# Performance work log

Hardware: AMD Instinct MI355X
Metric: run time of the kernel (lower is better)

The kernel has to match this reference:

```python
import jax, jax.numpy as jnp
from jax import lax
import numpy as np

# Keras LSTM cell semantics: gate order [i, f, c(candidate), o];
# recurrent_activation = sigmoid, activation = act (relu for all layers except
# the final decoder LSTM which uses tanh). h = o * act(c).

def lstm_layer(x, W, U, b, act, return_sequences):
    # x: [B, T, I], W: [I, 4H], U: [H, 4H], b: [4H]
    B = x.shape[0]
    H = U.shape[0]
    xW = jnp.einsum('bti,ih->bth', x, W) + b  # precompute input projections
    def step(carry, xw_t):
        h, c = carry
        z = xw_t + h @ U                      # [B, 4H]
        i, f, g, o = jnp.split(z, 4, axis=-1)
        i = jax.nn.sigmoid(i)
        f = jax.nn.sigmoid(f)
        g = act(g)
        o = jax.nn.sigmoid(o)
        c = f * c + i * g
        h = o * act(c)
        return (h, c), h
    h0 = jnp.zeros((B, H), x.dtype)
    (hT, _), hs = lax.scan(step, (h0, h0), jnp.swapaxes(xW, 0, 1))
    if return_sequences:
        return jnp.swapaxes(hs, 0, 1)         # [B, T, H]
    return hT                                  # [B, H]

# layer dims: (in, hidden) for enc0, enc1, enc_latent, dec0, dec1, dec_out
LAYER_DIMS = [(256, 512), (512, 256), (256, 64), (64, 256), (256, 512), (512, 256)]

def setup_inputs() -> dict:
    key = jax.random.key(0)
    keys = jax.random.split(key, 1 + 3 * len(LAYER_DIMS))
    inp = {'x': jax.random.normal(keys[0], (64, 256, 256), dtype=jnp.float32)}
    for li, (din, dh) in enumerate(LAYER_DIMS):
        kw, ku, _ = keys[1 + 3 * li], keys[2 + 3 * li], keys[3 + 3 * li]
        sW = 1.0 / np.sqrt(din)
        sU = 1.0 / np.sqrt(dh)
        inp[f'W{li}'] = jax.random.normal(kw, (din, 4 * dh), dtype=jnp.float32) * sW
        inp[f'U{li}'] = jax.random.normal(ku, (dh, 4 * dh), dtype=jnp.float32) * sU
        inp[f'b{li}'] = jnp.zeros((4 * dh,), dtype=jnp.float32)
    return inp

def reference(x, W0, U0, b0, W1, U1, b1, W2, U2, b2, W3, U3, b3, W4, U4, b4, W5, U5, b5):
    relu = jax.nn.relu
    # encoder: relu LSTMs, all return_sequences=True
    h = lstm_layer(x, W0, U0, b0, relu, True)
    h = lstm_layer(h, W1, U1, b1, relu, True)
    h = lstm_layer(h, W2, U2, b2, relu, True)   # latent_dim=64
    # decoder: relu LSTMs then final tanh LSTM with return_sequences=False
    h = lstm_layer(h, W3, U3, b3, relu, True)
    h = lstm_layer(h, W4, U4, b4, relu, True)
    out = lstm_layer(h, W5, U5, b5, jnp.tanh, False)  # [B, input_size]
    return out
```

## Files before the change

kernel.cpp:

```cpp
#include <hip/hip_runtime.h>
#include <stdint.h>

#define AGENT __HIP_MEMORY_SCOPE_AGENT
typedef unsigned long long u64;

__global__ __launch_bounds__(256) void xpose_in(const float* __restrict__ x,
                                                float* __restrict__ xT) {
  const int t = blockIdx.x;
  const int b = threadIdx.x & 63;
  const int w = threadIdx.x >> 6;
  const float* xr = x + ((size_t)b * 256 + t) * 256;
  float* o = xT + (size_t)t * 256 * 64;
  for (int kq = w * 16; kq < w * 16 + 16; ++kq) {
    float4 v = *(const float4*)(xr + kq * 4);
    o[(size_t)(kq * 4 + 0) * 64 + b] = v.x;
    o[(size_t)(kq * 4 + 1) * 64 + b] = v.y;
    o[(size_t)(kq * 4 + 2) * 64 + b] = v.z;
    o[(size_t)(kq * 4 + 3) * 64 + b] = v.w;
  }
}

__global__ __launch_bounds__(256) void pack_wu(const float* __restrict__ W,
                                               const float* __restrict__ U,
                                               float* __restrict__ out,
                                               int DIN, int H) {
  __shared__ float tile[64][65];
  const int KT = DIN + H;
  const int KTq = KT >> 2;
  const int c0 = blockIdx.x * 64;
  const int k0 = blockIdx.y * 64;
  const int tx = threadIdx.x & 63;
  const int ty = threadIdx.x >> 6;
  for (int r = ty; r < 64; r += 4) {
    const int k = k0 + r;
    tile[r][tx] = (k < DIN) ? W[(size_t)k * (4 * H) + c0 + tx]
                            : U[(size_t)(k - DIN) * (4 * H) + c0 + tx];
  }
  __syncthreads();
  for (int r = ty; r < 64; r += 4) {
    const int cg = c0 + r;
    const int g = cg / H;
    const int col = cg - g * H;
    const int wg = col >> 2;
    const int jl = col & 3;
    const int c = (g << 2) | jl;
    const int k = k0 + tx;
    const int q = k >> 2;
    const int j = k & 3;
    out[(((size_t)wg * KTq + q) * 16 + c) * 4 + j] = tile[tx][r];
  }
}

#define SB __builtin_amdgcn_sched_barrier(0)
#define FMA_K4(A_, W_, M_)                                            \
  A_ = fmaf((W_).x, x0_.M_, A_); A_ = fmaf((W_).y, x1_.M_, A_);       \
  A_ = fmaf((W_).z, x2_.M_, A_); A_ = fmaf((W_).w, x3_.M_, A_);
#define FMA_ROW16(W_, O_)      \
  FMA_K4(acc[(O_) + 0], W_, x) \
  FMA_K4(acc[(O_) + 1], W_, y) \
  FMA_K4(acc[(O_) + 2], W_, z) \
  FMA_K4(acc[(O_) + 3], W_, w)

template <int QW>
__device__ __forceinline__ void accum_cb(const float4* __restrict__ src4,
                                         const float4* __restrict__ wl4,
                                         int bq, int cq4, float acc[16]) {
  static_assert(QW % 4 == 0, "grouping assumes 4|QW");
#pragma unroll 1
  for (int g = 0; g < QW; g += 4) {
#pragma unroll
    for (int ql = g; ql < g + 4; ++ql) {
      const float4 x0_ = src4[(size_t)ql * 64 + 0 * 16 + bq];
      const float4 x1_ = src4[(size_t)ql * 64 + 1 * 16 + bq];
      const float4 x2_ = src4[(size_t)ql * 64 + 2 * 16 + bq];
      const float4 x3_ = src4[(size_t)ql * 64 + 3 * 16 + bq];
      const float4 w0_ = wl4[ql * 16 + cq4 + 0];
      const float4 w1_ = wl4[ql * 16 + cq4 + 1];
      const float4 w2_ = wl4[ql * 16 + cq4 + 2];
      const float4 w3_ = wl4[ql * 16 + cq4 + 3];
      FMA_ROW16(w0_, 0)
      FMA_ROW16(w1_, 4)
      FMA_ROW16(w2_, 8)
      FMA_ROW16(w3_, 12)
    }
    SB;
  }
}

template <int NWG>
__device__ __forceinline__ void agg_body(unsigned* __restrict__ flg,
                                         unsigned* __restrict__ ep) {
  const int tid = threadIdx.x;
  if (tid >= 64) return;
  for (int t = 0; t < 256; ++t) {
    unsigned* base = flg + (size_t)t * NWG;
    if (NWG <= 64) {
      if (tid < NWG) {
        while (__hip_atomic_load(base + tid, __ATOMIC_RELAXED, AGENT) == 0u)
          __builtin_amdgcn_s_sleep(1);
      }
    } else {
      while (__hip_atomic_load(base + tid, __ATOMIC_RELAXED, AGENT) == 0u)
        __builtin_amdgcn_s_sleep(1);
      while (__hip_atomic_load(base + 64 + tid, __ATOMIC_RELAXED, AGENT) == 0u)
        __builtin_amdgcn_s_sleep(1);
    }
    asm volatile("s_waitcnt vmcnt(0)" ::: "memory");
    if (tid == 0)
      __hip_atomic_store(ep, (unsigned)(t + 1), __ATOMIC_RELAXED, AGENT);
  }
}

template <int DIN, int H, int NWG, bool FIN, bool XCOH>
__device__ __forceinline__ void layer_body(
    int wg, int tid, const float* __restrict__ xin, float* __restrict__ hseq,
    const float* __restrict__ wP, const float* __restrict__ bias,
    float* __restrict__ dout, unsigned* __restrict__ selfF,
    unsigned* __restrict__ selfE, unsigned* __restrict__ prevE,
    float* __restrict__ wL, float (*sZ)[16][64], float* sH) {
  constexpr int KT = DIN + H;
  constexpr int KTq = KT / 4;
  constexpr int QX = DIN / 16;
  constexpr int QH = H / 16;
  constexpr int T = 256;
  static_assert(QX % 4 == 0 && QH % 4 == 0, "grouping assumes 4|QW");

  const int lane = tid & 63;
  const int wv = tid >> 6;
  const int bq = lane & 15;
  const int cq4 = (lane >> 4) * 4;

  {
    float4* wl = (float4*)wL;
    const float4* wp = (const float4*)wP + (size_t)wg * KTq * 16;
    for (int i = tid; i < KTq * 16; i += 256) wl[i] = wp[i];
  }
  const float4* wl4x = (const float4*)wL + (size_t)wv * QX * 16;
  const float4* wl4h = (const float4*)wL + ((size_t)(DIN / 4) + wv * QH) * 16;

  float bz[4];
#pragma unroll
  for (int g = 0; g < 4; ++g) bz[g] = bias[g * H + wg * 4 + wv];
  float cst = 0.f;
  __syncthreads();

  for (int t = 0; t < T; ++t) {
    float acc[16];
#pragma unroll
    for (int c = 0; c < 16; ++c) acc[c] = 0.f;

    if (!XCOH) {
      accum_cb<QX>((const float4*)(xin + (size_t)t * DIN * 64) +
                       (size_t)wv * QX * 64,
                   wl4x, bq, cq4, acc);
    }
    if (t > 0 && tid == 0) {
      while (__hip_atomic_load(selfE, __ATOMIC_RELAXED, AGENT) < (unsigned)t)
        __builtin_amdgcn_s_sleep(2);
    }
    if (XCOH && tid == 64) {
      while (__hip_atomic_load(prevE, __ATOMIC_RELAXED, AGENT) <
             (unsigned)(t + 1))
        __builtin_amdgcn_s_sleep(2);
    }
    __syncthreads();
    asm volatile("" ::: "memory");

    if (XCOH) {
      accum_cb<QX>((const float4*)(xin + (size_t)t * DIN * 64) +
                       (size_t)wv * QX * 64,
                   wl4x, bq, cq4, acc);
    }
    if (t > 0) {
      accum_cb<QH>((const float4*)(hseq + (size_t)(t - 1) * H * 64) +
                       (size_t)wv * QH * 64,
                   wl4h, bq, cq4, acc);
    }

#pragma unroll
    for (int i = 0; i < 4; ++i) {
      *(float4*)&sZ[wv][cq4 + i][bq * 4] = make_float4(
          acc[i * 4 + 0], acc[i * 4 + 1], acc[i * 4 + 2], acc[i * 4 + 3]);
    }
    __syncthreads();

    float z[4];
#pragma unroll
    for (int g = 0; g < 4; ++g) {
      z[g] = bz[g];
#pragma unroll
      for (int k = 0; k < 4; ++k) z[g] += sZ[k][g * 4 + wv][lane];
    }
    const float ig = 1.f / (1.f + __expf(-z[0]));
    const float fg = 1.f / (1.f + __expf(-z[1]));
    const float gg = FIN ? tanhf(z[2]) : fmaxf(z[2], 0.f);
    const float og = 1.f / (1.f + __expf(-z[3]));
    cst = fg * cst + ig * gg;
    const float ca = FIN ? tanhf(cst) : fmaxf(cst, 0.f);
    const float h = og * ca;
    sH[lane * 4 + wv] = h;
    if (FIN && t == T - 1) dout[(size_t)lane * H + wg * 4 + wv] = h;
    __syncthreads();

    if (wv == 0) {
      float* hw = hseq + (size_t)t * H * 64 + (size_t)(wg * 4) * 64 + lane;
#pragma unroll
      for (int jl = 0; jl < 4; ++jl) {
        __hip_atomic_store(hw + jl * 64, sH[lane * 4 + jl], __ATOMIC_RELAXED,
                           AGENT);
      }
      asm volatile("s_waitcnt vmcnt(0)" ::: "memory");
      if (tid == 0)
        __hip_atomic_store(&selfF[t * NWG + wg], 1u, __ATOMIC_RELAXED, AGENT);
    }
  }
}

__global__ __launch_bounds__(256, 2) void lstm_fused(
    const float* __restrict__ xT, float* __restrict__ h0,
    float* __restrict__ h1, float* __restrict__ h2, float* __restrict__ h3,
    float* __restrict__ h4, float* __restrict__ h5,
    const float* __restrict__ wuT0, const float* __restrict__ wuT1,
    const float* __restrict__ wuT2, const float* __restrict__ wuT3,
    const float* __restrict__ wuT4, const float* __restrict__ wuT5,
    const float* __restrict__ b0, const float* __restrict__ b1,
    const float* __restrict__ b2, const float* __restrict__ b3,
    const float* __restrict__ b4, const float* __restrict__ b5,
    float* __restrict__ dout, unsigned* __restrict__ f0,
    unsigned* __restrict__ f1, unsigned* __restrict__ f2,
    unsigned* __restrict__ f3, unsigned* __restrict__ f4,
    unsigned* __restrict__ f5, unsigned* __restrict__ eps) {
  __shared__ alignas(16) float wLDS[16 * 768];
  __shared__ alignas(16) float sZ[4][16][64];
  __shared__ alignas(16) float sH[256];
  const int b = blockIdx.x;
  const int tid = threadIdx.x;
  if (b < 128) {
    layer_body<256, 512, 128, false, false>(b, tid, xT, h0, wuT0, b0, nullptr,
                                            f0, eps + 0, nullptr, wLDS, sZ, sH);
  } else if (b < 256) {
    layer_body<256, 512, 128, false, true>(b - 128, tid, h3, h4, wuT4, b4,
                                           nullptr, f4, eps + 4, eps + 3, wLDS,
                                           sZ, sH);
  } else if (b < 320) {
    layer_body<512, 256, 64, false, true>(b - 256, tid, h0, h1, wuT1, b1,
                                          nullptr, f1, eps + 1, eps + 0, wLDS,
                                          sZ, sH);
  } else if (b < 384) {
    layer_body<64, 256, 64, false, true>(b - 320, tid, h2, h3, wuT3, b3,
                                         nullptr, f3, eps + 3, eps + 2, wLDS,
                                         sZ, sH);
  } else if (b < 448) {
    layer_body<512, 256, 64, true, true>(b - 384, tid, h4, h5, wuT5, b5, dout,
                                         f5, eps + 5, eps + 4, wLDS, sZ, sH);
  } else if (b < 464) {
    layer_body<256, 64, 16, false, true>(b - 448, tid, h1, h2, wuT2, b2,
                                         nullptr, f2, eps + 2, eps + 1, wLDS,
                                         sZ, sH);
  } else {
    const int l = b - 464;
    if (l == 0) agg_body<128>(f0, eps + 0);
    else if (l == 1) agg_body<64>(f1, eps + 1);
    else if (l == 2) agg_body<16>(f2, eps + 2);
    else if (l == 3) agg_body<64>(f3, eps + 3);
    else if (l == 4) agg_body<128>(f4, eps + 4);
    else agg_body<64>(f5, eps + 5);
  }
}

extern "C" void kernel_launch(void* const* d_in, const int* in_sizes, int n_in,
                              void* d_out, int out_size, void* d_ws,
                              size_t ws_size, hipStream_t stream) {
  (void)in_sizes; (void)n_in; (void)out_size; (void)ws_size;
  const float* x = (const float*)d_in[0];
  const float* W[6];
  const float* U[6];
  const float* B[6];
  for (int l = 0; l < 6; ++l) {
    W[l] = (const float*)d_in[1 + 3 * l];
    U[l] = (const float*)d_in[2 + 3 * l];
    B[l] = (const float*)d_in[3 + 3 * l];
  }
  char* ws = (char*)d_ws;
  unsigned* f0 = (unsigned*)ws;
  unsigned* f1 = f0 + 128 * 256;
  unsigned* f2 = f1 + 64 * 256;
  unsigned* f3 = f2 + 16 * 256;
  unsigned* f4 = f3 + 64 * 256;
  unsigned* f5 = f4 + 128 * 256;
  unsigned* eps = f0 + 464 * 256;
  float* wuT0 = (float*)(ws + (1u << 20));
  float* wuT1 = wuT0 + (size_t)2048 * 768;
  float* wuT2 = wuT1 + (size_t)1024 * 768;
  float* wuT3 = wuT2 + (size_t)256 * 320;
  float* wuT4 = wuT3 + (size_t)1024 * 320;
  float* wuT5 = wuT4 + (size_t)2048 * 768;
  float* xT = (float*)(ws + (22u << 20));
  float* h0 = (float*)(ws + (38u << 20));
  float* h1 = (float*)(ws + (70u << 20));
  float* h2 = (float*)(ws + (86u << 20));
  float* h3 = (float*)(ws + (90u << 20));
  float* h4 = (float*)(ws + (106u << 20));
  float* h5 = (float*)(ws + (138u << 20));

  hipMemsetAsync(f0, 0, (464 * 256 + 8) * sizeof(unsigned), stream);
  xpose_in<<<256, 256, 0, stream>>>(x, xT);
  pack_wu<<<dim3(32, 12), 256, 0, stream>>>(W[0], U[0], wuT0, 256, 512);
  pack_wu<<<dim3(16, 12), 256, 0, stream>>>(W[1], U[1], wuT1, 512, 256);
  pack_wu<<<dim3(4, 5), 256, 0, stream>>>(W[2], U[2], wuT2, 256, 64);
  pack_wu<<<dim3(16, 5), 256, 0, stream>>>(W[3], U[3], wuT3, 64, 256);
  pack_wu<<<dim3(32, 12), 256, 0, stream>>>(W[4], U[4], wuT4, 256, 512);
  pack_wu<<<dim3(16, 12), 256, 0, stream>>>(W[5], U[5], wuT5, 512, 256);

  lstm_fused<<<470, 256, 0, stream>>>(xT, h0, h1, h2, h3, h4, h5, wuT0, wuT1,
                                      wuT2, wuT3, wuT4, wuT5, B[0], B[1], B[2],
                                      B[3], B[4], B[5], (float*)d_out, f0, f1,
                                      f2, f3, f4, f5, eps);
}
```

Measured before the change: 3.826 ms.

## Double-buffer loads in the accumulation loop and split waits for cross-layer input

```diff
diff --git a/kernel.cpp b/kernel.cpp
--- a/kernel.cpp
+++ b/kernel.cpp
@@ -61,28 +61,46 @@
   FMA_K4(acc[(O_) + 2], W_, z) \
   FMA_K4(acc[(O_) + 3], W_, w)
 
+#define PFX(XB_, S_)                                                      \
+  {                                                                       \
+    _Pragma("unroll") for (int j_ = 0; j_ < 8; ++j_)                      \
+        XB_[j_] =                                                         \
+        src4[(size_t)((S_)*2 + (j_ >> 2)) * 64 + (j_ & 3) * 16 + bq];     \
+  }
+#define PFW(WB_, S_)                                                      \
+  {                                                                       \
+    _Pragma("unroll") for (int j_ = 0; j_ < 8; ++j_)                      \
+        WB_[j_] = wl4[((S_)*2 + (j_ >> 2)) * 16 + cq4 + (j_ & 3)];        \
+  }
+#define FMA2Q(XB_, WB_)                                                   \
+  {                                                                       \
+    {                                                                     \
+      const float4 x0_ = XB_[0], x1_ = XB_[1], x2_ = XB_[2], x3_ = XB_[3];\
+      FMA_ROW16(WB_[0], 0) FMA_ROW16(WB_[1], 4)                           \
+      FMA_ROW16(WB_[2], 8) FMA_ROW16(WB_[3], 12)                          \
+    }                                                                     \
+    {                                                                     \
+      const float4 x0_ = XB_[4], x1_ = XB_[5], x2_ = XB_[6], x3_ = XB_[7];\
+      FMA_ROW16(WB_[4], 0) FMA_ROW16(WB_[5], 4)                           \
+      FMA_ROW16(WB_[6], 8) FMA_ROW16(WB_[7], 12)                          \
+    }                                                                     \
+  }
+
 template <int QW>
 __device__ __forceinline__ void accum_cb(const float4* __restrict__ src4,
                                          const float4* __restrict__ wl4,
                                          int bq, int cq4, float acc[16]) {
-  static_assert(QW % 4 == 0, "grouping assumes 4|QW");
+  static_assert(QW % 4 == 0, "pipeline assumes 4|QW");
+  constexpr int NS = QW / 2;
+  float4 X0[8], X1[8], W0[8], W1[8];
+  PFX(X0, 0) PFW(W0, 0)
 #pragma unroll 1
-  for (int g = 0; g < QW; g += 4) {
-#pragma unroll
-    for (int ql = g; ql < g + 4; ++ql) {
-      const float4 x0_ = src4[(size_t)ql * 64 + 0 * 16 + bq];
-      const float4 x1_ = src4[(size_t)ql * 64 + 1 * 16 + bq];
-      const float4 x2_ = src4[(size_t)ql * 64 + 2 * 16 + bq];
-      const float4 x3_ = src4[(size_t)ql * 64 + 3 * 16 + bq];
-      const float4 w0_ = wl4[ql * 16 + cq4 + 0];
-      const float4 w1_ = wl4[ql * 16 + cq4 + 1];
-      const float4 w2_ = wl4[ql * 16 + cq4 + 2];
-      const float4 w3_ = wl4[ql * 16 + cq4 + 3];
-      FMA_ROW16(w0_, 0)
-      FMA_ROW16(w1_, 4)
-      FMA_ROW16(w2_, 8)
-      FMA_ROW16(w3_, 12)
-    }
+  for (int s = 0; s < NS; s += 2) {
+    PFX(X1, s + 1) PFW(W1, s + 1)
+    FMA2Q(X0, W0)
+    SB;
+    if (s + 2 < NS) { PFX(X0, s + 2) PFW(W0, s + 2) }
+    FMA2Q(X1, W1)
     SB;
   }
 }
@@ -123,7 +141,7 @@
   constexpr int QX = DIN / 16;
   constexpr int QH = H / 16;
   constexpr int T = 256;
-  static_assert(QX % 4 == 0 && QH % 4 == 0, "grouping assumes 4|QW");
+  static_assert(QX % 4 == 0 && QH % 4 == 0, "pipeline assumes 4|QW");
 
   const int lane = tid & 63;
   const int wv = tid >> 6;
@@ -153,24 +171,31 @@
       accum_cb<QX>((const float4*)(xin + (size_t)t * DIN * 64) +
                        (size_t)wv * QX * 64,
                    wl4x, bq, cq4, acc);
-    }
-    if (t > 0 && tid == 0) {
-      while (__hip_atomic_load(selfE, __ATOMIC_RELAXED, AGENT) < (unsigned)t)
-        __builtin_amdgcn_s_sleep(2);
-    }
-    if (XCOH && tid == 64) {
-      while (__hip_atomic_load(prevE, __ATOMIC_RELAXED, AGENT) <
-             (unsigned)(t + 1))
-        __builtin_amdgcn_s_sleep(2);
-    }
-    __syncthreads();
-    asm volatile("" ::: "memory");
-
-    if (XCOH) {
+      if (t > 0 && tid == 0) {
+        while (__hip_atomic_load(selfE, __ATOMIC_RELAXED, AGENT) < (unsigned)t)
+          __builtin_amdgcn_s_sleep(2);
+      }
+      __syncthreads();
+      asm volatile("" ::: "memory");
+    } else {
+      if (tid == 64) {
+        while (__hip_atomic_load(prevE, __ATOMIC_RELAXED, AGENT) <
+               (unsigned)(t + 1))
+          __builtin_amdgcn_s_sleep(2);
+      }
+      __syncthreads();
+      asm volatile("" ::: "memory");
       accum_cb<QX>((const float4*)(xin + (size_t)t * DIN * 64) +
                        (size_t)wv * QX * 64,
                    wl4x, bq, cq4, acc);
-    }
+      if (t > 0 && tid == 0) {
+        while (__hip_atomic_load(selfE, __ATOMIC_RELAXED, AGENT) < (unsigned)t)
+          __builtin_amdgcn_s_sleep(2);
+      }
+      __syncthreads();
+      asm volatile("" ::: "memory");
+    }
+
     if (t > 0) {
       accum_cb<QH>((const float4*)(hseq + (size_t)(t - 1) * H * 64) +
                        (size_t)wv * QH * 64,
```

Measured after the change: 4.079 ms. 6.6% more time.

## Split the per-step K reduction across eight waves with 512-thread blocks

Applied to the files above, without the earlier changes.

```diff
diff --git a/kernel.cpp b/kernel.cpp
--- a/kernel.cpp
+++ b/kernel.cpp
@@ -65,11 +65,12 @@
 __device__ __forceinline__ void accum_cb(const float4* __restrict__ src4,
                                          const float4* __restrict__ wl4,
                                          int bq, int cq4, float acc[16]) {
-  static_assert(QW % 4 == 0, "grouping assumes 4|QW");
+  constexpr int G = (QW % 4 == 0) ? 4 : 2;
+  static_assert(QW % G == 0, "");
 #pragma unroll 1
-  for (int g = 0; g < QW; g += 4) {
-#pragma unroll
-    for (int ql = g; ql < g + 4; ++ql) {
+  for (int g = 0; g < QW; g += G) {
+#pragma unroll
+    for (int ql = g; ql < g + G; ++ql) {
       const float4 x0_ = src4[(size_t)ql * 64 + 0 * 16 + bq];
       const float4 x1_ = src4[(size_t)ql * 64 + 1 * 16 + bq];
       const float4 x2_ = src4[(size_t)ql * 64 + 2 * 16 + bq];
@@ -120,27 +121,29 @@
     float* __restrict__ wL, float (*sZ)[16][64], float* sH) {
   constexpr int KT = DIN + H;
   constexpr int KTq = KT / 4;
-  constexpr int QX = DIN / 16;
-  constexpr int QH = H / 16;
+  constexpr int QX = DIN / 32;
+  constexpr int QH = H / 32;
   constexpr int T = 256;
-  static_assert(QX % 4 == 0 && QH % 4 == 0, "grouping assumes 4|QW");
+  static_assert(QX == 2 || QX % 4 == 0, "");
+  static_assert(QH == 2 || QH % 4 == 0, "");
 
   const int lane = tid & 63;
   const int wv = tid >> 6;
+  const int jw = wv & 3;
   const int bq = lane & 15;
   const int cq4 = (lane >> 4) * 4;
 
   {
     float4* wl = (float4*)wL;
     const float4* wp = (const float4*)wP + (size_t)wg * KTq * 16;
-    for (int i = tid; i < KTq * 16; i += 256) wl[i] = wp[i];
+    for (int i = tid; i < KTq * 16; i += 512) wl[i] = wp[i];
   }
   const float4* wl4x = (const float4*)wL + (size_t)wv * QX * 16;
   const float4* wl4h = (const float4*)wL + ((size_t)(DIN / 4) + wv * QH) * 16;
 
   float bz[4];
 #pragma unroll
-  for (int g = 0; g < 4; ++g) bz[g] = bias[g * H + wg * 4 + wv];
+  for (int g = 0; g < 4; ++g) bz[g] = bias[g * H + wg * 4 + jw];
   float cst = 0.f;
   __syncthreads();
 
@@ -177,29 +180,45 @@
                    wl4h, bq, cq4, acc);
     }
 
-#pragma unroll
-    for (int i = 0; i < 4; ++i) {
-      *(float4*)&sZ[wv][cq4 + i][bq * 4] = make_float4(
-          acc[i * 4 + 0], acc[i * 4 + 1], acc[i * 4 + 2], acc[i * 4 + 3]);
+    if (wv < 4) {
+#pragma unroll
+      for (int i = 0; i < 4; ++i) {
+        *(float4*)&sZ[wv][cq4 + i][bq * 4] = make_float4(
+            acc[i * 4 + 0], acc[i * 4 + 1], acc[i * 4 + 2], acc[i * 4 + 3]);
+      }
     }
     __syncthreads();
-
-    float z[4];
-#pragma unroll
-    for (int g = 0; g < 4; ++g) {
-      z[g] = bz[g];
-#pragma unroll
-      for (int k = 0; k < 4; ++k) z[g] += sZ[k][g * 4 + wv][lane];
-    }
-    const float ig = 1.f / (1.f + __expf(-z[0]));
-    const float fg = 1.f / (1.f + __expf(-z[1]));
-    const float gg = FIN ? tanhf(z[2]) : fmaxf(z[2], 0.f);
-    const float og = 1.f / (1.f + __expf(-z[3]));
-    cst = fg * cst + ig * gg;
-    const float ca = FIN ? tanhf(cst) : fmaxf(cst, 0.f);
-    const float h = og * ca;
-    sH[lane * 4 + wv] = h;
-    if (FIN && t == T - 1) dout[(size_t)lane * H + wg * 4 + wv] = h;
+    if (wv >= 4) {
+#pragma unroll
+      for (int i = 0; i < 4; ++i) {
+        float4 v = *(const float4*)&sZ[wv - 4][cq4 + i][bq * 4];
+        v.x += acc[i * 4 + 0];
+        v.y += acc[i * 4 + 1];
+        v.z += acc[i * 4 + 2];
+        v.w += acc[i * 4 + 3];
+        *(float4*)&sZ[wv - 4][cq4 + i][bq * 4] = v;
+      }
+    }
+    __syncthreads();
+
+    if (wv < 4) {
+      float z[4];
+#pragma unroll
+      for (int g = 0; g < 4; ++g) {
+        z[g] = bz[g];
+#pragma unroll
+        for (int k = 0; k < 4; ++k) z[g] += sZ[k][g * 4 + jw][lane];
+      }
+      const float ig = 1.f / (1.f + __expf(-z[0]));
+      const float fg = 1.f / (1.f + __expf(-z[1]));
+      const float gg = FIN ? tanhf(z[2]) : fmaxf(z[2], 0.f);
+      const float og = 1.f / (1.f + __expf(-z[3]));
+      cst = fg * cst + ig * gg;
+      const float ca = FIN ? tanhf(cst) : fmaxf(cst, 0.f);
+      const float h = og * ca;
+      sH[lane * 4 + jw] = h;
+      if (FIN && t == T - 1) dout[(size_t)lane * H + wg * 4 + jw] = h;
+    }
     __syncthreads();
 
     if (wv == 0) {
@@ -216,7 +235,7 @@
   }
 }
 
-__global__ __launch_bounds__(256, 2) void lstm_fused(
+__global__ __launch_bounds__(512, 4) void lstm_fused(
     const float* __restrict__ xT, float* __restrict__ h0,
     float* __restrict__ h1, float* __restrict__ h2, float* __restrict__ h3,
     float* __restrict__ h4, float* __restrict__ h5,
@@ -312,7 +331,7 @@
   pack_wu<<<dim3(32, 12), 256, 0, stream>>>(W[4], U[4], wuT4, 256, 512);
   pack_wu<<<dim3(16, 12), 256, 0, stream>>>(W[5], U[5], wuT5, 512, 256);
 
-  lstm_fused<<<470, 256, 0, stream>>>(xT, h0, h1, h2, h3, h4, h5, wuT0, wuT1,
+  lstm_fused<<<470, 512, 0, stream>>>(xT, h0, h1, h2, h3, h4, h5, wuT0, wuT1,
                                       wuT2, wuT3, wuT4, wuT5, B[0], B[1], B[2],
                                       B[3], B[4], B[5], (float*)d_out, f0, f1,
                                       f2, f3, f4, f5, eps);
```

Measured after the change: 4.405 ms. 15.1% more time.

## Stage activation chunks into LDS via async global_load_lds triple buffering

Applied to the files above, without the earlier changes.

```diff
diff --git a/kernel.cpp b/kernel.cpp
--- a/kernel.cpp
+++ b/kernel.cpp
@@ -61,29 +61,60 @@
   FMA_K4(acc[(O_) + 2], W_, z) \
   FMA_K4(acc[(O_) + 3], W_, w)
 
+typedef const __attribute__((address_space(1))) void* gas_t;
+typedef __attribute__((address_space(3))) void* las_t;
+#define GLDS(G_, L_) \
+  __builtin_amdgcn_global_load_lds((gas_t)(const void*)(G_), \
+                                   (las_t)(void*)(L_), 16, 0, 0)
+#define STAGE2(C_, P_)                                            \
+  {                                                               \
+    const float4* g_ = src4 + (size_t)(C_)*128 + lane;            \
+    float* l_ = xb + (P_)*512;                                    \
+    GLDS(g_, l_);                                                 \
+    GLDS(g_ + 64, l_ + 256);                                      \
+  }
+
 template <int QW>
-__device__ __forceinline__ void accum_cb(const float4* __restrict__ src4,
-                                         const float4* __restrict__ wl4,
-                                         int bq, int cq4, float acc[16]) {
-  static_assert(QW % 4 == 0, "grouping assumes 4|QW");
+__device__ __forceinline__ void accum_lds(const float4* __restrict__ src4,
+                                          float* __restrict__ xb,
+                                          const float4* __restrict__ wl4,
+                                          int lane, int bq, int cq4,
+                                          float acc[16]) {
+  static_assert(QW % 2 == 0 && QW >= 4, "");
+  constexpr int NC = QW / 2;
+  STAGE2(0, 0)
+  STAGE2(1, 1)
+  int pc = 0, pn = 2;
 #pragma unroll 1
-  for (int g = 0; g < QW; g += 4) {
-#pragma unroll
-    for (int ql = g; ql < g + 4; ++ql) {
-      const float4 x0_ = src4[(size_t)ql * 64 + 0 * 16 + bq];
-      const float4 x1_ = src4[(size_t)ql * 64 + 1 * 16 + bq];
-      const float4 x2_ = src4[(size_t)ql * 64 + 2 * 16 + bq];
-      const float4 x3_ = src4[(size_t)ql * 64 + 3 * 16 + bq];
-      const float4 w0_ = wl4[ql * 16 + cq4 + 0];
-      const float4 w1_ = wl4[ql * 16 + cq4 + 1];
-      const float4 w2_ = wl4[ql * 16 + cq4 + 2];
-      const float4 w3_ = wl4[ql * 16 + cq4 + 3];
+  for (int c = 0; c < NC; ++c) {
+    if (c + 2 < NC) {
+      STAGE2(c + 2, pn)
+      asm volatile("s_waitcnt vmcnt(4)" ::: "memory");
+    } else {
+      asm volatile("s_waitcnt vmcnt(0)" ::: "memory");
+    }
+    SB;
+    const float4* wq_ = wl4 + (size_t)c * 32;
+    const float* xc_ = xb + pc * 512;
+#pragma unroll
+    for (int q = 0; q < 2; ++q) {
+      const float4* xq_ = (const float4*)(xc_ + q * 256);
+      const float4 x0_ = xq_[0 + bq];
+      const float4 x1_ = xq_[16 + bq];
+      const float4 x2_ = xq_[32 + bq];
+      const float4 x3_ = xq_[48 + bq];
+      const float4 w0_ = wq_[q * 16 + cq4 + 0];
+      const float4 w1_ = wq_[q * 16 + cq4 + 1];
+      const float4 w2_ = wq_[q * 16 + cq4 + 2];
+      const float4 w3_ = wq_[q * 16 + cq4 + 3];
       FMA_ROW16(w0_, 0)
       FMA_ROW16(w1_, 4)
       FMA_ROW16(w2_, 8)
       FMA_ROW16(w3_, 12)
     }
     SB;
+    pc = (pc == 2) ? 0 : pc + 1;
+    pn = (pn == 2) ? 0 : pn + 1;
   }
 }
 
@@ -117,18 +148,20 @@
     const float* __restrict__ wP, const float* __restrict__ bias,
     float* __restrict__ dout, unsigned* __restrict__ selfF,
     unsigned* __restrict__ selfE, unsigned* __restrict__ prevE,
-    float* __restrict__ wL, float (*sZ)[16][64], float* sH) {
+    float* __restrict__ wL, float* __restrict__ xU, float* sH) {
   constexpr int KT = DIN + H;
   constexpr int KTq = KT / 4;
   constexpr int QX = DIN / 16;
   constexpr int QH = H / 16;
   constexpr int T = 256;
-  static_assert(QX % 4 == 0 && QH % 4 == 0, "grouping assumes 4|QW");
+  static_assert(QX % 2 == 0 && QH % 2 == 0, "");
 
   const int lane = tid & 63;
   const int wv = tid >> 6;
   const int bq = lane & 15;
   const int cq4 = (lane >> 4) * 4;
+  float (*sZ)[16][64] = (float(*)[16][64])xU;
+  float* xb = xU + (size_t)wv * 1536;
 
   {
     float4* wl = (float4*)wL;
@@ -150,9 +183,9 @@
     for (int c = 0; c < 16; ++c) acc[c] = 0.f;
 
     if (!XCOH) {
-      accum_cb<QX>((const float4*)(xin + (size_t)t * DIN * 64) +
-                       (size_t)wv * QX * 64,
-                   wl4x, bq, cq4, acc);
+      accum_lds<QX>((const float4*)(xin + (size_t)t * DIN * 64) +
+                        (size_t)wv * QX * 64,
+                    xb, wl4x, lane, bq, cq4, acc);
     }
     if (t > 0 && tid == 0) {
       while (__hip_atomic_load(selfE, __ATOMIC_RELAXED, AGENT) < (unsigned)t)
@@ -167,16 +200,17 @@
     asm volatile("" ::: "memory");
 
     if (XCOH) {
-      accum_cb<QX>((const float4*)(xin + (size_t)t * DIN * 64) +
-                       (size_t)wv * QX * 64,
-                   wl4x, bq, cq4, acc);
+      accum_lds<QX>((const float4*)(xin + (size_t)t * DIN * 64) +
+                        (size_t)wv * QX * 64,
+                    xb, wl4x, lane, bq, cq4, acc);
     }
     if (t > 0) {
-      accum_cb<QH>((const float4*)(hseq + (size_t)(t - 1) * H * 64) +
-                       (size_t)wv * QH * 64,
-                   wl4h, bq, cq4, acc);
-    }
-
+      accum_lds<QH>((const float4*)(hseq + (size_t)(t - 1) * H * 64) +
+                        (size_t)wv * QH * 64,
+                    xb, wl4h, lane, bq, cq4, acc);
+    }
+
+    __syncthreads();
 #pragma unroll
     for (int i = 0; i < 4; ++i) {
       *(float4*)&sZ[wv][cq4 + i][bq * 4] = make_float4(
@@ -231,32 +265,32 @@
     unsigned* __restrict__ f3, unsigned* __restrict__ f4,
     unsigned* __restrict__ f5, unsigned* __restrict__ eps) {
   __shared__ alignas(16) float wLDS[16 * 768];
-  __shared__ alignas(16) float sZ[4][16][64];
+  __shared__ alignas(16) float xU[4 * 3 * 512];
   __shared__ alignas(16) float sH[256];
   const int b = blockIdx.x;
   const int tid = threadIdx.x;
   if (b < 128) {
     layer_body<256, 512, 128, false, false>(b, tid, xT, h0, wuT0, b0, nullptr,
-                                            f0, eps + 0, nullptr, wLDS, sZ, sH);
+                                            f0, eps + 0, nullptr, wLDS, xU, sH);
   } else if (b < 256) {
     layer_body<256, 512, 128, false, true>(b - 128, tid, h3, h4, wuT4, b4,
                                            nullptr, f4, eps + 4, eps + 3, wLDS,
-                                           sZ, sH);
+                                           xU, sH);
   } else if (b < 320) {
     layer_body<512, 256, 64, false, true>(b - 256, tid, h0, h1, wuT1, b1,
                                           nullptr, f1, eps + 1, eps + 0, wLDS,
-                                          sZ, sH);
+                                          xU, sH);
   } else if (b < 384) {
     layer_body<64, 256, 64, false, true>(b - 320, tid, h2, h3, wuT3, b3,
                                          nullptr, f3, eps + 3, eps + 2, wLDS,
-                                         sZ, sH);
+                                         xU, sH);
   } else if (b < 448) {
     layer_body<512, 256, 64, true, true>(b - 384, tid, h4, h5, wuT5, b5, dout,
-                                         f5, eps + 5, eps + 4, wLDS, sZ, sH);
+                                         f5, eps + 5, eps + 4, wLDS, xU, sH);
   } else if (b < 464) {
     layer_body<256, 64, 16, false, true>(b - 448, tid, h1, h2, wuT2, b2,
                                          nullptr, f2, eps + 2, eps + 1, wLDS,
-                                         sZ, sH);
+                                         xU, sH);
   } else {
     const int l = b - 464;
     if (l == 0) agg_body<128>(f0, eps + 0);
```

After: 4.079 ms. 6.6% more time.
